# Performance work log

Measured on AMD Instinct MI355X. Metric: run time of the kernel, lower is better.

Reference implementation:

```python
import jax, jax.numpy as jnp
import numpy as np

D_MODEL, D_INNER, D_CONV, D_STATE, DT_RANK = 1024, 2048, 4, 16, 64
ALPHA, CHUNK = 0.1, 64


def setup_inputs() -> dict:
    key = jax.random.key(0)
    ks = jax.random.split(key, 10)
    B, T = 2, 2048
    s = lambda k, shape, scale: jax.random.normal(k, shape, jnp.float32) * scale
    return {
        "x": s(ks[0], (B, T, D_MODEL), 1.0),
        "norm1_w": jnp.ones((D_MODEL,), jnp.float32),
        "norm2_w": jnp.ones((D_MODEL,), jnp.float32),
        "in_proj_w": s(ks[1], (2 * D_INNER, D_MODEL), 0.02),
        "in_proj_b": jnp.zeros((2 * D_INNER,), jnp.float32),
        "conv_w": s(ks[2], (D_INNER, 1, D_CONV), 0.1),
        "conv_b": jnp.zeros((D_INNER,), jnp.float32),
        "x_proj_w": s(ks[3], (DT_RANK + 2 * D_STATE, D_INNER), 0.02),
        "dt_proj_w": s(ks[4], (D_INNER, DT_RANK), 0.02),
        "dt_proj_b": s(ks[5], (D_INNER,), 0.02),
        "A_log": jnp.log(jnp.broadcast_to(jnp.arange(1, D_STATE + 1, dtype=jnp.float32), (D_INNER, D_STATE))) + 0.0,
        "D_ssm": jnp.ones((D_INNER,), jnp.float32),
        "out_proj_w": s(ks[6], (D_MODEL, D_INNER), 0.02),
        "out_proj_b": jnp.zeros((D_MODEL,), jnp.float32),
        "proj_write_w": s(ks[7], (D_MODEL, D_MODEL), 0.02),
        "proj_read_w": s(ks[8], (D_MODEL, D_MODEL), 0.02),
        "decay": jnp.float32(4.6),
    }


def rmsnorm(x, w, eps=1e-5):
    return x * jax.lax.rsqrt(jnp.mean(x * x, axis=-1, keepdims=True) + eps) * w


def mamba_block(x, in_w, in_b, conv_w, conv_b, xp_w, dt_w, dt_b, A_log, D_ssm, out_w, out_b):
    # canonical (mamba-minimal) selective-SSM block
    B, T, _ = x.shape
    xz = x @ in_w.T + in_b                      # (B,T,2*d_inner)
    xm, res = jnp.split(xz, 2, axis=-1)
    # causal depthwise conv over time
    xc = jax.lax.conv_general_dilated(
        xm.transpose(0, 2, 1), conv_w, (1,), [(D_CONV - 1, 0)],
        dimension_numbers=("NCH", "OIH", "NCH"), feature_group_count=D_INNER)
    xm = jax.nn.silu(xc.transpose(0, 2, 1) + conv_b)
    x_dbl = xm @ xp_w.T                         # (B,T,dt_rank+2*d_state)
    delta = jax.nn.softplus(x_dbl[..., :DT_RANK] @ dt_w.T + dt_b)
    Bm = x_dbl[..., DT_RANK:DT_RANK + D_STATE]
    Cm = x_dbl[..., DT_RANK + D_STATE:]
    A = -jnp.exp(A_log)                          # (d_inner, d_state)

    def step(h, ins):
        d_t, B_t, C_t, u_t = ins                 # (B,di),(B,ds),(B,ds),(B,di)
        dA = jnp.exp(d_t[:, :, None] * A)
        h = h * dA + (d_t * u_t)[:, :, None] * B_t[:, None, :]
        y = jnp.einsum("bds,bs->bd", h, C_t)
        return h, y

    h0 = jnp.zeros((B, D_INNER, D_STATE), x.dtype)
    _, ys = jax.lax.scan(step, h0, (delta.transpose(1, 0, 2), Bm.transpose(1, 0, 2),
                                    Cm.transpose(1, 0, 2), xm.transpose(1, 0, 2)))
    y = ys.transpose(1, 0, 2) + xm * D_ssm
    y = y * jax.nn.silu(res)
    return y @ out_w.T + out_b


def memory_attend(out, w_write, w_read, decay):
    # chunked Hebbian write/read (RetNet-style chunked linear attention)
    B, T, D = out.shape
    C = CHUNK
    gamma = jax.nn.sigmoid(decay)
    log_gamma = jnp.log(gamma)
    v = out @ w_write.T
    wk = jnp.pad(out[:, :-1], ((0, 0), (1, 0), (0, 0)))
    rk = out
    n = T // C
    p = jnp.arange(C)
    diffs = jnp.clip(p[:, None] - 1 - p[None, :], 0, None).astype(out.dtype)
    causal = (p[:, None] > p[None, :]).astype(out.dtype)
    M = jnp.exp(diffs * log_gamma) * causal      # (C,C) intra-chunk decay mask
    g_in = gamma ** p                            # (C,)
    g_w = gamma ** (C - 1 - p)                   # (C,)

    chunked = lambda a: a.reshape(B, n, C, D).transpose(1, 0, 2, 3)  # (n,B,C,D)

    def step(W, ins):
        rk_c, wk_c, v_c = ins                    # each (B,C,D)
        inter = jnp.einsum("bde,bce->bcd", W, rk_c) * g_in[None, :, None]
        S = jnp.einsum("bcd,bkd->bck", rk_c, wk_c)
        intra = jnp.einsum("bck,bkd->bcd", S * M, v_c)
        W_new = (gamma ** C) * W + jnp.einsum("bcd,bce->bde", v_c * g_w[None, :, None], wk_c)
        return W_new, inter + intra

    W0 = jnp.zeros((B, D, D), out.dtype)
    _, reads = jax.lax.scan(step, W0, (chunked(rk), chunked(wk), chunked(v)))
    reads = reads.transpose(1, 0, 2, 3).reshape(B, T, D)
    return out + ALPHA * (reads @ w_read.T)


def reference(x, norm1_w, norm2_w, in_proj_w, in_proj_b, conv_w, conv_b, x_proj_w,
              dt_proj_w, dt_proj_b, A_log, D_ssm, out_proj_w, out_proj_b,
              proj_write_w, proj_read_w, decay):
    mb = lambda h: mamba_block(h, in_proj_w, in_proj_b, conv_w, conv_b, x_proj_w,
                               dt_proj_w, dt_proj_b, A_log, D_ssm, out_proj_w, out_proj_b)
    out1 = mb(rmsnorm(x, norm1_w))
    x1 = x + out1
    out2 = mb(rmsnorm(x1, norm2_w))   # tied weights: same params as mamba1
    out2 = memory_attend(out2, proj_write_w, proj_read_w, decay)
    return x1 + out2
```

## Files before the change

### kernel.cpp

```cpp
#include <hip/hip_runtime.h>
#include <hip/hip_bf16.h>
#include <math.h>

typedef __hip_bfloat16 bf16;
typedef __attribute__((ext_vector_type(4))) float f32x4;
typedef __attribute__((ext_vector_type(8))) short bf16x8;
typedef __attribute__((ext_vector_type(8))) unsigned short u16x8;

static __device__ __forceinline__ float b2f(bf16 v) { return __bfloat162float(v); }
static __device__ __forceinline__ float us2f(unsigned short u) {
  union { unsigned short s; bf16 h; } c; c.s = u; return __bfloat162float(c.h);
}
static __device__ __forceinline__ void  stv(float* p, float v) { *p = v; }
static __device__ __forceinline__ void  stv(bf16* p, float v) { *p = __float2bfloat16(v); }
static __device__ __forceinline__ float ldin(const void* p, size_t i, int f) {
  return f ? ((const float*)p)[i] : b2f(((const bf16*)p)[i]);
}
static __device__ __forceinline__ unsigned short f2b(float x) {
  bf16 h = __float2bfloat16(x);
  return *reinterpret_cast<unsigned short*>(&h);
}

static __device__ __forceinline__ void gl16(const unsigned short* g,
                                            void* ldsbase, int byteoff) {
  __builtin_amdgcn_global_load_lds(
      (const __attribute__((address_space(1))) unsigned int*)g,
      (__attribute__((address_space(3))) unsigned int*)((char*)ldsbase + byteoff),
      16, 0, 0);
}

constexpr int B_  = 2;
constexpr int T_  = 2048;
constexpr int DM  = 1024;
constexpr int DI  = 2048;
constexpr int DS  = 16;
constexpr int DTR = 64;
constexpr int ROWS = B_ * T_;
constexpr int SL  = 32;
constexpr int NSC = T_ / SL;
constexpr int KSP = 4;

__global__ void detect_k(const void* __restrict__ decay, int* __restrict__ flag) {
  flag[0] = (((const unsigned short*)decay)[0] == 0x4093) ? 0 : 1;
  flag[1] = 0;
}

__global__ void sentinel_k(void* __restrict__ out, float val, int n,
                           const int* __restrict__ df) {
  int f = *df;
  int i = blockIdx.x * 256 + threadIdx.x;
  if (i < n) {
    if (f) ((float*)out)[i] = val;
    else   ((bf16*)out)[i] = __float2bfloat16(val);
  }
}

__global__ void cvt1_k(const void* __restrict__ src, bf16* __restrict__ dst, int n,
                       const int* __restrict__ df) {
  int f = *df;
  int i = blockIdx.x * 256 + threadIdx.x;
  if (i < n) stv(&dst[i], ldin(src, i, f));
}

__global__ void rmsnorm_k(const void* __restrict__ xin, const void* __restrict__ w,
                          bf16* __restrict__ out, const int* __restrict__ df,
                          int xin_raw) {
  int f = *df;
  int fx = xin_raw ? f : 0;
  int row = blockIdx.x;
  int tid = threadIdx.x;
  float ss = 0.f;
  for (int d = tid; d < DM; d += 256) {
    float v = ldin(xin, (size_t)row * DM + d, fx);
    ss += v * v;
  }
  for (int o = 32; o > 0; o >>= 1) ss += __shfl_down(ss, o, 64);
  __shared__ float sred[4];
  int lane = tid & 63, wid = tid >> 6;
  if (lane == 0) sred[wid] = ss;
  __syncthreads();
  if (tid == 0) {
    float t = sred[0] + sred[1] + sred[2] + sred[3];
    sred[0] = 1.f / sqrtf(t / DM + 1e-5f);
  }
  __syncthreads();
  float rs = sred[0];
  for (int d = tid; d < DM; d += 256) {
    float v = ldin(xin, (size_t)row * DM + d, fx);
    stv(&out[(size_t)row * DM + d], v * rs * ldin(w, d, f));
  }
}

__global__ void transpose_k(const bf16* __restrict__ src, bf16* __restrict__ dst) {
  __shared__ unsigned short tile[64][65];
  int b = blockIdx.z;
  int t0 = blockIdx.x * 64, d0 = blockIdx.y * 64;
  int tid = threadIdx.x;
  int lt = tid & 63, lq = tid >> 6;
  const unsigned short* sp = (const unsigned short*)src;
  unsigned short* dp = (unsigned short*)dst;
#pragma unroll
  for (int i = 0; i < 16; i++) {
    int r = lq * 16 + i;
    tile[r][lt] = sp[((size_t)b * T_ + t0 + r) * DM + d0 + lt];
  }
  __syncthreads();
#pragma unroll
  for (int i = 0; i < 16; i++) {
    int r = lq * 16 + i;
    dp[((size_t)b * DM + d0 + r) * T_ + t0 + lt] = tile[lt][r];
  }
}

__global__ __launch_bounds__(512, 2)
void gemm256_k(const bf16* __restrict__ A, int lda,
               const void* __restrict__ B, int ldb,
               const void* __restrict__ bias,
               bf16* __restrict__ C, int ldc, int K,
               const int* __restrict__ df) {
  __shared__ alignas(16) unsigned char smem[65536];
  int f = *df;
  int m0 = blockIdx.y * 256, n0 = blockIdx.x * 256;
  int tid = threadIdx.x;
  int wave = tid >> 6, lane = tid & 63, quad = lane >> 4, l15 = lane & 15;
  int wrow = wave >> 2, wcol = wave & 3;
  const unsigned short* Ag = (const unsigned short*)A;
  const unsigned short* Bg = (const unsigned short*)B;
  f32x4 acc[8][4] = {};

  int r0 = tid >> 2;
  int kc = (((tid & 3) ^ ((r0 >> 1) & 3))) * 8;
  int xq = (quad ^ ((l15 >> 1) & 3)) * 16;

  auto stg = [&](int t, int isB, int dd) {
    const unsigned short* src = isB ? Bg : Ag;
    int ld = isB ? ldb : lda;
    int x0 = isB ? n0 : m0;
    int rbase = (isB ? 32768 : 0) + dd * 16384;
    int kk = t * 32;
    gl16(src + (size_t)(x0 + r0) * ld + kk + kc, smem, rbase + wave * 1024);
    gl16(src + (size_t)(x0 + r0 + 128) * ld + kk + kc, smem,
         rbase + 8192 + wave * 1024);
  };
  auto rdA = [&](int dd, int fr) {
    return *(const bf16x8*)(smem + dd * 16384 + wrow * 8192 + fr * 1024 +
                            l15 * 64 + xq);
  };
  auto rdB = [&](int dd, int fc) {
    return *(const bf16x8*)(smem + 32768 + dd * 16384 + wcol * 4096 +
                            fc * 1024 + l15 * 64 + xq);
  };

  int NT = K >> 5;
  if (f) {
    for (int t = 0; t < NT; ++t) {
      stg(t, 0, 0);
      {
        int r = tid >> 1, h = (tid & 1) * 16;
        const float* bp = (const float*)B + (size_t)(n0 + r) * ldb + t * 32 + h;
        float4 x0 = *(const float4*)bp,       x1 = *(const float4*)(bp + 4);
        float4 x2 = *(const float4*)(bp + 8), x3 = *(const float4*)(bp + 12);
        union { unsigned short s[8]; uint4 v; } p0, p1;
        p0.s[0]=f2b(x0.x); p0.s[1]=f2b(x0.y); p0.s[2]=f2b(x0.z); p0.s[3]=f2b(x0.w);
        p0.s[4]=f2b(x1.x); p0.s[5]=f2b(x1.y); p0.s[6]=f2b(x1.z); p0.s[7]=f2b(x1.w);
        p1.s[0]=f2b(x2.x); p1.s[1]=f2b(x2.y); p1.s[2]=f2b(x2.z); p1.s[3]=f2b(x2.w);
        p1.s[4]=f2b(x3.x); p1.s[5]=f2b(x3.y); p1.s[6]=f2b(x3.z); p1.s[7]=f2b(x3.w);
        int rx = (r >> 1) & 3;
        int c0 = (tid & 1) * 2;
        *(uint4*)(smem + 32768 + r * 64 + ((c0 ^ rx) * 16))       = p0.v;
        *(uint4*)(smem + 32768 + r * 64 + (((c0 + 1) ^ rx) * 16)) = p1.v;
      }
      __syncthreads();
      bf16x8 af[8], bv0, bv1, bv2, bv3;
#pragma unroll
      for (int fr = 0; fr < 8; fr++) af[fr] = rdA(0, fr);
      bv0 = rdB(0, 0); bv1 = rdB(0, 1); bv2 = rdB(0, 2); bv3 = rdB(0, 3);
#pragma unroll
      for (int fr = 0; fr < 8; fr++) {
        acc[fr][0] = __builtin_amdgcn_mfma_f32_16x16x32_bf16(af[fr], bv0, acc[fr][0], 0, 0, 0);
        acc[fr][1] = __builtin_amdgcn_mfma_f32_16x16x32_bf16(af[fr], bv1, acc[fr][1], 0, 0, 0);
        acc[fr][2] = __builtin_amdgcn_mfma_f32_16x16x32_bf16(af[fr], bv2, acc[fr][2], 0, 0, 0);
        acc[fr][3] = __builtin_amdgcn_mfma_f32_16x16x32_bf16(af[fr], bv3, acc[fr][3], 0, 0, 0);
      }
      __syncthreads();
    }
  } else {
    stg(0, 0, 0); stg(0, 1, 0);
    stg(1, 0, 1);
    asm volatile("s_waitcnt vmcnt(2)" ::: "memory");
    __builtin_amdgcn_sched_barrier(0);
    __builtin_amdgcn_s_barrier();
    for (int t = 0; t < NT; ++t) {
      int d = t & 1;
      bf16x8 af[8], bv0, bv1;
#pragma unroll
      for (int fr = 0; fr < 8; fr++) af[fr] = rdA(d, fr);
      bv0 = rdB(d, 0); bv1 = rdB(d, 1);
      if (t + 1 < NT) stg(t + 1, 1, d ^ 1);
      __builtin_amdgcn_s_barrier();
      asm volatile("s_waitcnt lgkmcnt(0)" ::: "memory");
      __builtin_amdgcn_sched_barrier(0);
      __builtin_amdgcn_s_setprio(1);
#pragma unroll
      for (int fr = 0; fr < 8; fr++) {
        acc[fr][0] = __builtin_amdgcn_mfma_f32_16x16x32_bf16(af[fr], bv0, acc[fr][0], 0, 0, 0);
        acc[fr][1] = __builtin_amdgcn_mfma_f32_16x16x32_bf16(af[fr], bv1, acc[fr][1], 0, 0, 0);
      }
      __builtin_amdgcn_s_setprio(0);
      __builtin_amdgcn_s_barrier();
      bf16x8 bv2, bv3;
      bv2 = rdB(d, 2); bv3 = rdB(d, 3);
      if (t + 2 < NT) stg(t + 2, 0, d);
      __builtin_amdgcn_s_barrier();
      asm volatile("s_waitcnt lgkmcnt(0)" ::: "memory");
      __builtin_amdgcn_sched_barrier(0);
      __builtin_amdgcn_s_setprio(1);
#pragma unroll
      for (int fr = 0; fr < 8; fr++) {
        acc[fr][2] = __builtin_amdgcn_mfma_f32_16x16x32_bf16(af[fr], bv2, acc[fr][2], 0, 0, 0);
        acc[fr][3] = __builtin_amdgcn_mfma_f32_16x16x32_bf16(af[fr], bv3, acc[fr][3], 0, 0, 0);
      }
      __builtin_amdgcn_s_setprio(0);
      if (t + 1 < NT) {
        if (t + 2 < NT)
          asm volatile("s_waitcnt vmcnt(2)" ::: "memory");
        else
          asm volatile("s_waitcnt vmcnt(0)" ::: "memory");
        __builtin_amdgcn_sched_barrier(0);
        __builtin_amdgcn_s_barrier();
      }
    }
  }

#pragma unroll
  for (int fr = 0; fr < 8; fr++) {
#pragma unroll
    for (int rr = 0; rr < 4; rr++) {
      int row = m0 + wrow * 128 + fr * 16 + quad * 4 + rr;
#pragma unroll
      for (int fc = 0; fc < 4; fc++) {
        int col = n0 + wcol * 64 + fc * 16 + l15;
        float v = acc[fr][fc][rr];
        if (bias) v += ldin(bias, col, f);
        C[(size_t)row * ldc + col] = __float2bfloat16(v);
      }
    }
  }
}

template <int MODE, int ACT, int MROWS>
__global__ void mgemm_k(const bf16* __restrict__ A, size_t sAz, int lda,
                        const void* __restrict__ B, size_t sBz, int ldb,
                        const void* __restrict__ bias,
                        bf16* __restrict__ C, size_t sCz, int ldc,
                        int M, int N, int K,
                        const void* __restrict__ dec, const int* __restrict__ df) {
  constexpr int FR = MROWS / 32;
  int by = (MODE == 2) ? ((int)gridDim.y - 1 - (int)blockIdx.y) : (int)blockIdx.y;
  int m0 = by * MROWS, n0 = blockIdx.x * 128;
  if (MODE == 1 && n0 > m0 + MROWS - 1) return;
  int f = *df;
  int bz = blockIdx.z;
  const bf16* Ab = A + (size_t)bz * sAz;
  const unsigned short* Bb16 =
      (const unsigned short*)B + (size_t)bz * sBz;
  bf16* Cb = C + (size_t)bz * sCz;
  int kmax = (MODE == 2) ? (m0 + MROWS) : K;
  __shared__ alignas(16) unsigned short As[2][MROWS][32];
  __shared__ alignas(16) unsigned short Bs[2][128][32];
  int tid = threadIdx.x;
  int wave = tid >> 6, lane = tid & 63, quad = lane >> 4, l15 = lane & 15;
  int wr = (wave >> 1) * (MROWS / 2), wc = (wave & 1) * 64;
  f32x4 acc[FR][4] = {};
  int lrow = lane >> 2;
  int lh = (((lane & 3) ^ ((lrow >> 1) & 3))) * 8;
  int xqs = (quad ^ ((l15 >> 1) & 3)) * 8;
  const unsigned short* Aus = (const unsigned short*)Ab;

  auto stage = [&](int buf, int k0) {
    if (MROWS == 128) {
#pragma unroll
      for (int q = 0; q < 2; q++) {
        int seg = wave * 2 + q;
        int rowa = seg * 16 + lrow;
        gl16(Aus + (size_t)(m0 + rowa) * lda + k0 + lh, &As[buf][0][0],
             seg * 1024);
      }
    } else {
      int rowa = wave * 16 + lrow;
      gl16(Aus + (size_t)(m0 + rowa) * lda + k0 + lh, &As[buf][0][0],
           wave * 1024);
    }
    if (MODE == 0 && f) {
      int r = tid >> 1, h = (tid & 1) * 16;
      const float* bp = (const float*)B + (size_t)(n0 + r) * ldb + k0 + h;
      float4 x0 = *(const float4*)bp,       x1 = *(const float4*)(bp + 4);
      float4 x2 = *(const float4*)(bp + 8), x3 = *(const float4*)(bp + 12);
      union { unsigned short s[8]; uint4 v; } p0, p1;
      p0.s[0]=f2b(x0.x); p0.s[1]=f2b(x0.y); p0.s[2]=f2b(x0.z); p0.s[3]=f2b(x0.w);
      p0.s[4]=f2b(x1.x); p0.s[5]=f2b(x1.y); p0.s[6]=f2b(x1.z); p0.s[7]=f2b(x1.w);
      p1.s[0]=f2b(x2.x); p1.s[1]=f2b(x2.y); p1.s[2]=f2b(x2.z); p1.s[3]=f2b(x2.w);
      p1.s[4]=f2b(x3.x); p1.s[5]=f2b(x3.y); p1.s[6]=f2b(x3.z); p1.s[7]=f2b(x3.w);
      int rx = (r >> 1) & 3;
      int c0 = (tid & 1) * 2;
      *(uint4*)&Bs[buf][r][(c0 ^ rx) * 8]       = p0.v;
      *(uint4*)&Bs[buf][r][((c0 + 1) ^ rx) * 8] = p1.v;
    } else {
#pragma unroll
      for (int q = 0; q < 2; q++) {
        int seg = wave * 2 + q;
        int rowb = seg * 16 + lrow;
        gl16(Bb16 + (size_t)(n0 + rowb) * ldb + k0 + lh, &Bs[buf][0][0],
             seg * 1024);
      }
    }
  };

  auto compute = [&](int buf) {
    bf16x8 af[FR], bfv[4];
#pragma unroll
    for (int i = 0; i < FR; i++)
      af[i] = *(const bf16x8*)&As[buf][wr + 16 * i + l15][xqs];
#pragma unroll
    for (int j = 0; j < 4; j++)
      bfv[j] = *(const bf16x8*)&Bs[buf][wc + 16 * j + l15][xqs];
#pragma unroll
    for (int i = 0; i < FR; i++)
#pragma unroll
      for (int j = 0; j < 4; j++)
        acc[i][j] = __builtin_amdgcn_mfma_f32_16x16x32_bf16(af[i], bfv[j],
                                                            acc[i][j], 0, 0, 0);
  };

  int nt = kmax >> 5;
  stage(0, 0);
  __syncthreads();
  int cur = 0;
  for (int t = 0; t < nt - 1; ++t) {
    stage(cur ^ 1, (t + 1) * 32);
    compute(cur);
    __syncthreads();
    cur ^= 1;
  }
  compute(cur);

  float lg = 0.f;
  if (MODE == 1) {
    float g = 1.f / (1.f + __expf(-ldin(dec, 0, f)));
    lg = __logf(g);
  }
#pragma unroll
  for (int i = 0; i < FR; i++) {
#pragma unroll
    for (int rr = 0; rr < 4; rr++) {
      int row = m0 + wr + 16 * i + quad * 4 + rr;
      if (MODE == 1 && n0 == 0 && wc == 0 && l15 == 0)
        Cb[(size_t)row * ldc] = __float2bfloat16(0.f);
#pragma unroll
      for (int j = 0; j < 4; j++) {
        int col = n0 + wc + 16 * j + l15;
        float v = acc[i][j][rr];
        if (MODE == 0) {
          if (bias) v += ldin(bias, col, f);
          if (ACT == 1) v = (v > 20.f) ? v : log1pf(__expf(v));
          Cb[(size_t)row * ldc + col] = __float2bfloat16(v);
        } else if (MODE == 1) {
          int colp = col + 1;
          int d_ = row - colp;
          v = (d_ > 0) ? v * __expf(lg * (float)(d_ - 1)) : 0.f;
          if (colp < N)
            Cb[(size_t)row * ldc + colp] = __float2bfloat16(v);
        } else {
          Cb[(size_t)row * ldc + col] = __float2bfloat16(v);
        }
      }
    }
  }
}

__global__ void conv_silu_k(const bf16* __restrict__ xz, const void* __restrict__ cw,
                            const void* __restrict__ cb, bf16* __restrict__ xm,
                            const int* __restrict__ df) {
  int f = *df;
  int i = blockIdx.x * 256 + threadIdx.x;
  int d = i & (DI - 1);
  int t = (i >> 11) & (T_ - 1);
  int b = i >> 22;
  const bf16* base = xz + (size_t)b * T_ * 2 * DI + d;
  float s = ldin(cb, d, f);
#pragma unroll
  for (int k = 0; k < 4; k++) {
    int tt = t - 3 + k;
    if (tt >= 0) s += ldin(cw, d * 4 + k, f) * b2f(base[(size_t)tt * 2 * DI]);
  }
  stv(&xm[i], s / (1.f + __expf(-s)));
}

__global__ void xproj_k(const bf16* __restrict__ xm, const void* __restrict__ xpw,
                        bf16* __restrict__ parts, const int* __restrict__ df) {
  int f = *df;
  int m0 = blockIdx.x * 128;
  int z = blockIdx.y;
  int kbase = z * (DI / KSP);
  __shared__ alignas(16) unsigned short As[2][128][32];
  __shared__ alignas(16) unsigned short Bs[2][96][32];
  int tid = threadIdx.x;
  int wave = tid >> 6, lane = tid & 63, quad = lane >> 4, l15 = lane & 15;
  int wr = wave * 32;
  f32x4 acc[2][6] = {};
  int lrow = lane >> 2;
  int lh = (((lane & 3) ^ ((lrow >> 1) & 3))) * 8;
  int xqs = (quad ^ ((l15 >> 1) & 3)) * 8;
  const unsigned short* Aus = (const unsigned short*)xm;
  const unsigned short* Bus = (const unsigned short*)xpw;

  auto stage = [&](int buf, int k0) {
#pragma unroll
    for (int q = 0; q < 2; q++) {
      int seg = wave * 2 + q;
      int rowa = seg * 16 + lrow;
      gl16(Aus + (size_t)(m0 + rowa) * DI + kbase + k0 + lh, &As[buf][0][0],
           seg * 1024);
    }
    if (f) {
      if (tid < 192) {
        int r2 = tid >> 1, h2 = (tid & 1) * 16;
        const float* bp = (const float*)xpw + (size_t)r2 * DI + kbase + k0 + h2;
        float4 x0 = *(const float4*)bp,       x1 = *(const float4*)(bp + 4);
        float4 x2 = *(const float4*)(bp + 8), x3 = *(const float4*)(bp + 12);
        union { unsigned short s[8]; uint4 v; } p0, p1;
        p0.s[0]=f2b(x0.x); p0.s[1]=f2b(x0.y); p0.s[2]=f2b(x0.z); p0.s[3]=f2b(x0.w);
        p0.s[4]=f2b(x1.x); p0.s[5]=f2b(x1.y); p0.s[6]=f2b(x1.z); p0.s[7]=f2b(x1.w);
        p1.s[0]=f2b(x2.x); p1.s[1]=f2b(x2.y); p1.s[2]=f2b(x2.z); p1.s[3]=f2b(x2.w);
        p1.s[4]=f2b(x3.x); p1.s[5]=f2b(x3.y); p1.s[6]=f2b(x3.z); p1.s[7]=f2b(x3.w);
        int rx = (r2 >> 1) & 3;
        int c0 = (tid & 1) * 2;
        *(uint4*)&Bs[buf][r2][(c0 ^ rx) * 8]       = p0.v;
        *(uint4*)&Bs[buf][r2][((c0 + 1) ^ rx) * 8] = p1.v;
      }
    } else if (wave < 3) {
#pragma unroll
      for (int q = 0; q < 2; q++) {
        int seg = wave * 2 + q;
        int rowb = seg * 16 + lrow;
        gl16(Bus + (size_t)rowb * DI + kbase + k0 + lh, &Bs[buf][0][0],
             seg * 1024);
      }
    }
  };

  auto compute = [&](int buf) {
    bf16x8 af[2], bfv[6];
#pragma unroll
    for (int i = 0; i < 2; i++)
      af[i] = *(const bf16x8*)&As[buf][wr + 16 * i + l15][xqs];
#pragma unroll
    for (int j = 0; j < 6; j++)
      bfv[j] = *(const bf16x8*)&Bs[buf][16 * j + l15][xqs];
#pragma unroll
    for (int i = 0; i < 2; i++)
#pragma unroll
      for (int j = 0; j < 6; j++)
        acc[i][j] = __builtin_amdgcn_mfma_f32_16x16x32_bf16(af[i], bfv[j],
                                                            acc[i][j], 0, 0, 0);
  };

  constexpr int NT = (DI / KSP) / 32;
  stage(0, 0);
  __syncthreads();
  int cur = 0;
  for (int t = 0; t < NT - 1; ++t) {
    stage(cur ^ 1, (t + 1) * 32);
    compute(cur);
    __syncthreads();
    cur ^= 1;
  }
  compute(cur);

  bf16* out = parts + (size_t)z * ROWS * 96;
#pragma unroll
  for (int i = 0; i < 2; i++)
#pragma unroll
    for (int rr = 0; rr < 4; rr++) {
      int row = m0 + wr + 16 * i + quad * 4 + rr;
#pragma unroll
      for (int j = 0; j < 6; j++) {
        int col = 16 * j + l15;
        out[(size_t)row * 96 + col] = __float2bfloat16(acc[i][j][rr]);
      }
    }
}

__global__ void reduce_xdbl_k(const bf16* __restrict__ parts, bf16* __restrict__ xdbl) {
  int i = blockIdx.x * 256 + threadIdx.x;
  if (i >= ROWS * 96) return;
  float s = 0.f;
#pragma unroll
  for (int z = 0; z < KSP; z++) s += b2f(parts[(size_t)z * ROWS * 96 + i]);
  stv(&xdbl[i], s);
}

__global__ void scan_p1_k(const bf16* __restrict__ delta, const bf16* __restrict__ xm,
                          const bf16* __restrict__ xdbl,
                          const void* __restrict__ alog,
                          bf16* __restrict__ F, float* __restrict__ S,
                          const int* __restrict__ df) {
  int f = *df;
  int idx = blockIdx.x * 256 + threadIdx.x;
  int d = idx & (DI - 1);
  int c = (idx >> 11) & (NSC - 1);
  int b = idx >> 17;
  float A[DS], hh[DS];
  bool fastA = true;
#pragma unroll
  for (int s = 0; s < DS; s++) {
    A[s] = -__expf(ldin(alog, d * DS + s, f));
    fastA = fastA && (fabsf(A[s] + (float)(s + 1)) < 1e-3f);
    hh[s] = 0.f;
  }
  int cs = c * SL;
  float ssum = 0.f;
  if (fastA) {
    for (int t = cs; t < cs + SL; t++) {
      size_t r = (size_t)b * T_ + t;
      float dlt = b2f(delta[r * DI + d]);
      float u = b2f(xm[r * DI + d]);
      ssum += dlt;
      float du = dlt * u;
      float q = __expf(-dlt);
      u16x8 t0 = *(const u16x8*)(xdbl + r * 96 + 64);
      u16x8 t1 = *(const u16x8*)(xdbl + r * 96 + 72);
      float e = 1.f;
#pragma unroll
      for (int s = 0; s < 8; s++) {
        e *= q; hh[s] = hh[s] * e + du * us2f(t0[s]);
      }
#pragma unroll
      for (int s = 0; s < 8; s++) {
        e *= q; hh[8 + s] = hh[8 + s] * e + du * us2f(t1[s]);
      }
    }
  } else {
    for (int t = cs; t < cs + SL; t++) {
      size_t r = (size_t)b * T_ + t;
      float dlt = b2f(delta[r * DI + d]);
      float u = b2f(xm[r * DI + d]);
      ssum += dlt;
      float du = dlt * u;
      u16x8 t0 = *(const u16x8*)(xdbl + r * 96 + 64);
      u16x8 t1 = *(const u16x8*)(xdbl + r * 96 + 72);
#pragma unroll
      for (int s = 0; s < 8; s++) {
        hh[s]     = hh[s]     * __expf(dlt * A[s])     + du * us2f(t0[s]);
        hh[8 + s] = hh[8 + s] * __expf(dlt * A[8 + s]) + du * us2f(t1[s]);
      }
    }
  }
#pragma unroll
  for (int s = 0; s < DS; s++) stv(&F[(size_t)idx * 16 + s], hh[s]);
  S[idx] = ssum;
}

__global__ void scan_p2_k(bf16* __restrict__ F, const float* __restrict__ S,
                          const void* __restrict__ alog, const int* __restrict__ df) {
  int f = *df;
  int idx = blockIdx.x * 256 + threadIdx.x;
  int s = idx & 15;
  int d = (idx >> 4) & (DI - 1);
  int b = idx >> 15;
  float As_ = -__expf(ldin(alog, d * DS + s, f));
  float H = 0.f;
  for (int c = 0; c < NSC; c++) {
    size_t base = (size_t)(b * NSC + c) * DI + d;
    float tmp = b2f(F[base * 16 + s]);
    stv(&F[base * 16 + s], H);
    H = __expf(As_ * S[base]) * H + tmp;
  }
}

__global__ void scan_p3_k(bf16* __restrict__ delta, const bf16* __restrict__ xm,
                          const bf16* __restrict__ xz, const bf16* __restrict__ xdbl,
                          const void* __restrict__ alog, const void* __restrict__ dssm,
                          const bf16* __restrict__ F, const int* __restrict__ df) {
  int f = *df;
  int idx = blockIdx.x * 256 + threadIdx.x;
  int d = idx & (DI - 1);
  int c = (idx >> 11) & (NSC - 1);
  int b = idx >> 17;
  float A[DS], hh[DS];
  bool fastA = true;
#pragma unroll
  for (int s = 0; s < DS; s++) {
    A[s] = -__expf(ldin(alog, d * DS + s, f));
    fastA = fastA && (fabsf(A[s] + (float)(s + 1)) < 1e-3f);
    hh[s] = b2f(F[(size_t)idx * 16 + s]);
  }
  float Dv = ldin(dssm, d, f);
  int cs = c * SL;
  if (fastA) {
    for (int t = cs; t < cs + SL; t++) {
      size_t r = (size_t)b * T_ + t;
      float dlt = b2f(delta[r * DI + d]);
      float u = b2f(xm[r * DI + d]);
      float du = dlt * u;
      float q = __expf(-dlt);
      u16x8 t0 = *(const u16x8*)(xdbl + r * 96 + 64);
      u16x8 t1 = *(const u16x8*)(xdbl + r * 96 + 72);
      u16x8 t2 = *(const u16x8*)(xdbl + r * 96 + 80);
      u16x8 t3 = *(const u16x8*)(xdbl + r * 96 + 88);
      float y = 0.f;
      float e = 1.f;
#pragma unroll
      for (int s = 0; s < 8; s++) {
        e *= q;
        hh[s] = hh[s] * e + du * us2f(t0[s]);
        y += hh[s] * us2f(t2[s]);
      }
#pragma unroll
      for (int s = 0; s < 8; s++) {
        e *= q;
        hh[8 + s] = hh[8 + s] * e + du * us2f(t1[s]);
        y += hh[8 + s] * us2f(t3[s]);
      }
      float res = b2f(xz[r * 2 * DI + DI + d]);
      y += u * Dv;
      y *= res / (1.f + __expf(-res));
      stv(&delta[r * DI + d], y);
    }
  } else {
    for (int t = cs; t < cs + SL; t++) {
      size_t r = (size_t)b * T_ + t;
      float dlt = b2f(delta[r * DI + d]);
      float u = b2f(xm[r * DI + d]);
      float du = dlt * u;
      u16x8 t0 = *(const u16x8*)(xdbl + r * 96 + 64);
      u16x8 t1 = *(const u16x8*)(xdbl + r * 96 + 72);
      u16x8 t2 = *(const u16x8*)(xdbl + r * 96 + 80);
      u16x8 t3 = *(const u16x8*)(xdbl + r * 96 + 88);
      float y = 0.f;
#pragma unroll
      for (int s = 0; s < 8; s++) {
        hh[s]     = hh[s]     * __expf(dlt * A[s])     + du * us2f(t0[s]);
        hh[8 + s] = hh[8 + s] * __expf(dlt * A[8 + s]) + du * us2f(t1[s]);
        y += hh[s] * us2f(t2[s]) + hh[8 + s] * us2f(t3[s]);
      }
      float res = b2f(xz[r * 2 * DI + DI + d]);
      y += u * Dv;
      y *= res / (1.f + __expf(-res));
      stv(&delta[r * DI + d], y);
    }
  }
}

__global__ void add_x1_k(const void* __restrict__ x, const bf16* __restrict__ o1,
                         bf16* __restrict__ x1, const int* __restrict__ df) {
  int f = *df;
  int i = blockIdx.x * 256 + threadIdx.x;
  if (i < ROWS * DM) stv(&x1[i], ldin(x, i, f) + b2f(o1[i]));
}

__global__ void final_k(const bf16* __restrict__ x1, const bf16* __restrict__ out2,
                        const bf16* __restrict__ rproj, void* __restrict__ out,
                        const int* __restrict__ df) {
  int f = *df;
  int i = blockIdx.x * 256 + threadIdx.x;
  if (i < ROWS * DM) {
    float v = b2f(x1[i]) + b2f(out2[i]) + 0.1f * b2f(rproj[i]);
    if (f) ((float*)out)[i] = v;
    else   stv(&((bf16*)out)[i], v);
  }
}

extern "C" void kernel_launch(void* const* d_in, const int* in_sizes, int n_in,
                              void* d_out, int out_size, void* d_ws, size_t ws_size,
                              hipStream_t stream) {
  (void)in_sizes; (void)n_in;
  const void* x    = d_in[0];
  const void* n1w  = d_in[1];
  const void* n2w  = d_in[2];
  const void* ipw  = d_in[3];
  const void* ipb  = d_in[4];
  const void* cw   = d_in[5];
  const void* cb   = d_in[6];
  const void* xpw  = d_in[7];
  const void* dtw  = d_in[8];
  const void* dtb  = d_in[9];
  const void* alog = d_in[10];
  const void* dssm = d_in[11];
  const void* opw  = d_in[12];
  const void* opb  = d_in[13];
  const void* pww  = d_in[14];
  const void* prw  = d_in[15];
  const void* dec  = d_in[16];

  char* base = (char*)d_ws;
  bf16*  xz    = (bf16*) (base + 0);
  bf16*  v     = (bf16*) (base + 0);
  bf16*  reads = (bf16*) (base + 8388608);
  bf16*  P     = (bf16*) (base + 16777216);
  bf16*  delta = (bf16*) (base + 33554432);
  bf16*  hnorm = delta;
  bf16*  rproj = (bf16*) (base + 33554432);
  bf16*  vt    = (bf16*) (base + 41943040);
  bf16*  xm    = (bf16*) (base + 50331648);
  bf16*  xdbl  = (bf16*) (base + 67108864);
  bf16*  parts = (bf16*) (base + 67895296);
  float* S     = (float*)(base + 67895296);
  bf16*  bout  = (bf16*) (base + 71041024);
  bf16*  F     = (bf16*) (base + 71041024);
  bf16*  x1    = (bf16*) (base + 79429632);
  int*   dflag = (int*)  (base + 87818240);
  bf16*  wbuf  = (bf16*) (base + 87818256);
  constexpr size_t WS_MIN = 87818248;
  constexpr int O_IPW = 0;
  constexpr int O_OPW = 4194304;
  constexpr int O_PWW = 6291456;
  constexpr int O_PRW = 7340032;
  constexpr int O_XPW = 8388608;
  constexpr int O_DTW = 8585216;
  constexpr int O_IPB = 8716288;
  constexpr int O_OPB = 8720384;
  constexpr int O_DTB = 8721408;
  constexpr int W_TOT = 8723456;
  constexpr size_t WS_BIG = 87818256 + (size_t)W_TOT * 2;

  detect_k<<<1, 1, 0, stream>>>(dec, dflag);
  if (ws_size < WS_MIN) {
    sentinel_k<<<(out_size + 255) / 256, 256, 0, stream>>>(
        d_out, (float)(ws_size >> 20), out_size, dflag);
    return;
  }

  const void *g_ipw = ipw, *g_ipb = ipb, *g_xpw = xpw, *g_dtw = dtw,
             *g_dtb = dtb, *g_opw = opw, *g_opb = opb, *g_pww = pww, *g_prw = prw;
  const int* wf = dflag;
  if (ws_size >= WS_BIG) {
    auto cvt = [&](const void* src, int off, int n) {
      cvt1_k<<<(n + 255) / 256, 256, 0, stream>>>(src, wbuf + off, n, dflag);
    };
    cvt(ipw, O_IPW, 4194304); cvt(opw, O_OPW, 2097152);
    cvt(pww, O_PWW, 1048576); cvt(prw, O_PRW, 1048576);
    cvt(xpw, O_XPW, 196608);  cvt(dtw, O_DTW, 131072);
    cvt(ipb, O_IPB, 4096);    cvt(opb, O_OPB, 1024);   cvt(dtb, O_DTB, 2048);
    g_ipw = wbuf + O_IPW; g_opw = wbuf + O_OPW; g_pww = wbuf + O_PWW;
    g_prw = wbuf + O_PRW; g_xpw = wbuf + O_XPW; g_dtw = wbuf + O_DTW;
    g_ipb = wbuf + O_IPB; g_opb = wbuf + O_OPB; g_dtb = wbuf + O_DTB;
    wf = dflag + 1;
  }

  auto mamba = [&](const void* xin, int xin_raw, const void* nw, bf16* outb) {
    rmsnorm_k<<<ROWS, 256, 0, stream>>>(xin, nw, hnorm, dflag, xin_raw);
    gemm256_k<<<dim3((2 * DI) / 256, ROWS / 256), 512, 0, stream>>>(
        hnorm, DM, g_ipw, DM, g_ipb, xz, 2 * DI, DM, wf);
    conv_silu_k<<<(ROWS * DI) / 256, 256, 0, stream>>>(xz, cw, cb, xm, dflag);
    xproj_k<<<dim3(32, KSP), 256, 0, stream>>>(xm, g_xpw, parts, wf);
    reduce_xdbl_k<<<(ROWS * 96) / 256, 256, 0, stream>>>(parts, xdbl);
    mgemm_k<0, 1, 128><<<dim3(16, 32, 1), 256, 0, stream>>>(
        xdbl, 0, 96, g_dtw, 0, DTR, g_dtb, delta, 0, DI, ROWS, DI, DTR, dec, wf);
    scan_p1_k<<<B_ * NSC * DI / 256, 256, 0, stream>>>(delta, xm, xdbl, alog, F, S, dflag);
    scan_p2_k<<<B_ * DI * 16 / 256, 256, 0, stream>>>(F, S, alog, dflag);
    scan_p3_k<<<B_ * NSC * DI / 256, 256, 0, stream>>>(delta, xm, xz, xdbl, alog, dssm, F, dflag);
    mgemm_k<0, 0, 64><<<dim3(8, 64, 1), 256, 0, stream>>>(
        delta, 0, DI, g_opw, 0, DI, g_opb, outb, 0, DM, ROWS, DM, DI, dec, wf);
  };

  mamba(x, 1, n1w, bout);
  add_x1_k<<<(ROWS * DM) / 256, 256, 0, stream>>>(x, bout, x1, dflag);
  mamba(x1, 0, n2w, bout);

  mgemm_k<0, 0, 64><<<dim3(8, 64, 1), 256, 0, stream>>>(
      bout, 0, DM, g_pww, 0, DM, nullptr, v, 0, DM, ROWS, DM, DM, dec, wf);
  transpose_k<<<dim3(T_ / 64, DM / 64, B_), 256, 0, stream>>>(v, vt);
  mgemm_k<1, 0, 64><<<dim3(16, 32, B_), 256, 0, stream>>>(
      bout, (size_t)T_ * DM, DM, bout, (size_t)T_ * DM, DM, nullptr,
      P, (size_t)T_ * T_, T_, T_, T_, DM, dec, dflag);
  mgemm_k<2, 0, 64><<<dim3(8, 32, B_), 256, 0, stream>>>(
      P, (size_t)T_ * T_, T_, vt, (size_t)DM * T_, T_, nullptr,
      reads, (size_t)T_ * DM, DM, T_, DM, T_, dec, dflag);
  mgemm_k<0, 0, 64><<<dim3(8, 64, 1), 256, 0, stream>>>(
      reads, 0, DM, g_prw, 0, DM, nullptr, rproj, 0, DM, ROWS, DM, DM, dec, wf);
  final_k<<<(ROWS * DM) / 256, 256, 0, stream>>>(x1, bout, rproj, d_out, dflag);
}
```

Baseline: 851.7 us.

## Deepen GEMM k-tile to 64 with four-phase staged LDS pipeline

```diff
diff --git a/kernel.cpp b/kernel.cpp
--- a/kernel.cpp
+++ b/kernel.cpp
@@ -118,7 +118,7 @@
                const void* __restrict__ bias,
                bf16* __restrict__ C, int ldc, int K,
                const int* __restrict__ df) {
-  __shared__ alignas(16) unsigned char smem[65536];
+  __shared__ alignas(16) unsigned char smem[131072];
   int f = *df;
   int m0 = blockIdx.y * 256, n0 = blockIdx.x * 256;
   int tid = threadIdx.x;
@@ -128,102 +128,167 @@
   const unsigned short* Bg = (const unsigned short*)B;
   f32x4 acc[8][4] = {};
 
-  int r0 = tid >> 2;
-  int kc = (((tid & 3) ^ ((r0 >> 1) & 3))) * 8;
-  int xq = (quad ^ ((l15 >> 1) & 3)) * 16;
-
-  auto stg = [&](int t, int isB, int dd) {
-    const unsigned short* src = isB ? Bg : Ag;
-    int ld = isB ? ldb : lda;
-    int x0 = isB ? n0 : m0;
-    int rbase = (isB ? 32768 : 0) + dd * 16384;
-    int kk = t * 32;
-    gl16(src + (size_t)(x0 + r0) * ld + kk + kc, smem, rbase + wave * 1024);
-    gl16(src + (size_t)(x0 + r0 + 128) * ld + kk + kc, smem,
-         rbase + 8192 + wave * 1024);
+  auto stgA = [&](int dbuf, int frh, int kstep) {
+#pragma unroll
+    for (int q = 0; q < 2; q++) {
+      int id = q * 512 + tid;
+      int rr8 = id >> 3;
+      int lc = (id & 7) ^ (rr8 & 7);
+      int wh = rr8 >> 6, rem = rr8 & 63;
+      int m = m0 + wh * 128 + frh * 64 + rem;
+      gl16(Ag + (size_t)m * lda + kstep * 64 + lc * 8, smem,
+           dbuf * 32768 + frh * 16384 + q * 8192 + wave * 1024);
+    }
   };
-  auto rdA = [&](int dd, int fr) {
-    return *(const bf16x8*)(smem + dd * 16384 + wrow * 8192 + fr * 1024 +
-                            l15 * 64 + xq);
+  auto stgB = [&](int dbuf, int fch, int kstep) {
+#pragma unroll
+    for (int q = 0; q < 2; q++) {
+      int id = q * 512 + tid;
+      int rr8 = id >> 3;
+      int lc = (id & 7) ^ (rr8 & 7);
+      int wc = rr8 >> 5, rem = rr8 & 31;
+      int n = n0 + wc * 64 + fch * 32 + rem;
+      gl16(Bg + (size_t)n * ldb + kstep * 64 + lc * 8, smem,
+           65536 + dbuf * 32768 + fch * 16384 + q * 8192 + wave * 1024);
+    }
   };
-  auto rdB = [&](int dd, int fc) {
-    return *(const bf16x8*)(smem + 32768 + dd * 16384 + wcol * 4096 +
-                            fc * 1024 + l15 * 64 + xq);
+  auto rdA = [&](int dbuf, int fr, int kk) {
+    int frh = fr >> 2, frl = fr & 3;
+    int phys = ((kk << 2) | quad) ^ (l15 & 7);
+    return *(const bf16x8*)(smem + dbuf * 32768 + frh * 16384 + wrow * 8192 +
+                            frl * 2048 + l15 * 128 + phys * 16);
   };
-
-  int NT = K >> 5;
+  auto rdB = [&](int dbuf, int fc, int kk) {
+    int fch = fc >> 1, fcl = fc & 1;
+    int phys = ((kk << 2) | quad) ^ (l15 & 7);
+    return *(const bf16x8*)(smem + 65536 + dbuf * 32768 + fch * 16384 +
+                            wcol * 4096 + fcl * 2048 + l15 * 128 + phys * 16);
+  };
+
+  int NT = K >> 6;
   if (f) {
     for (int t = 0; t < NT; ++t) {
-      stg(t, 0, 0);
-      {
-        int r = tid >> 1, h = (tid & 1) * 16;
-        const float* bp = (const float*)B + (size_t)(n0 + r) * ldb + t * 32 + h;
-        float4 x0 = *(const float4*)bp,       x1 = *(const float4*)(bp + 4);
-        float4 x2 = *(const float4*)(bp + 8), x3 = *(const float4*)(bp + 12);
-        union { unsigned short s[8]; uint4 v; } p0, p1;
-        p0.s[0]=f2b(x0.x); p0.s[1]=f2b(x0.y); p0.s[2]=f2b(x0.z); p0.s[3]=f2b(x0.w);
-        p0.s[4]=f2b(x1.x); p0.s[5]=f2b(x1.y); p0.s[6]=f2b(x1.z); p0.s[7]=f2b(x1.w);
-        p1.s[0]=f2b(x2.x); p1.s[1]=f2b(x2.y); p1.s[2]=f2b(x2.z); p1.s[3]=f2b(x2.w);
-        p1.s[4]=f2b(x3.x); p1.s[5]=f2b(x3.y); p1.s[6]=f2b(x3.z); p1.s[7]=f2b(x3.w);
-        int rx = (r >> 1) & 3;
-        int c0 = (tid & 1) * 2;
-        *(uint4*)(smem + 32768 + r * 64 + ((c0 ^ rx) * 16))       = p0.v;
-        *(uint4*)(smem + 32768 + r * 64 + (((c0 + 1) ^ rx) * 16)) = p1.v;
+      stgA(0, 0, t); stgA(0, 1, t);
+#pragma unroll
+      for (int c = 0; c < 4; c++) {
+        int id = tid * 4 + c;
+        int rr8 = id >> 3;
+        int p = id & 7;
+        int lc = p ^ (rr8 & 7);
+        int fch = rr8 >> 7, rl = rr8 & 127;
+        int wc = rl >> 5, rem = rl & 31;
+        int n = n0 + wc * 64 + fch * 32 + rem;
+        const float* bp = (const float*)B + (size_t)n * ldb + t * 64 + lc * 8;
+        union { unsigned short s[8]; uint4 v; } pk;
+#pragma unroll
+        for (int e = 0; e < 8; e++) pk.s[e] = f2b(bp[e]);
+        *(uint4*)(smem + 65536 + fch * 16384 + rl * 128 + p * 16) = pk.v;
       }
       __syncthreads();
-      bf16x8 af[8], bv0, bv1, bv2, bv3;
-#pragma unroll
-      for (int fr = 0; fr < 8; fr++) af[fr] = rdA(0, fr);
-      bv0 = rdB(0, 0); bv1 = rdB(0, 1); bv2 = rdB(0, 2); bv3 = rdB(0, 3);
 #pragma unroll
       for (int fr = 0; fr < 8; fr++) {
-        acc[fr][0] = __builtin_amdgcn_mfma_f32_16x16x32_bf16(af[fr], bv0, acc[fr][0], 0, 0, 0);
-        acc[fr][1] = __builtin_amdgcn_mfma_f32_16x16x32_bf16(af[fr], bv1, acc[fr][1], 0, 0, 0);
-        acc[fr][2] = __builtin_amdgcn_mfma_f32_16x16x32_bf16(af[fr], bv2, acc[fr][2], 0, 0, 0);
-        acc[fr][3] = __builtin_amdgcn_mfma_f32_16x16x32_bf16(af[fr], bv3, acc[fr][3], 0, 0, 0);
+        bf16x8 a0 = rdA(0, fr, 0), a1 = rdA(0, fr, 1);
+#pragma unroll
+        for (int fc = 0; fc < 4; fc++) {
+          acc[fr][fc] = __builtin_amdgcn_mfma_f32_16x16x32_bf16(
+              a0, rdB(0, fc, 0), acc[fr][fc], 0, 0, 0);
+          acc[fr][fc] = __builtin_amdgcn_mfma_f32_16x16x32_bf16(
+              a1, rdB(0, fc, 1), acc[fr][fc], 0, 0, 0);
+        }
       }
       __syncthreads();
     }
   } else {
-    stg(0, 0, 0); stg(0, 1, 0);
-    stg(1, 0, 1);
-    asm volatile("s_waitcnt vmcnt(2)" ::: "memory");
+    stgA(0, 0, 0); stgB(0, 0, 0); stgB(0, 1, 0); stgA(0, 1, 0);
+    if (NT > 1) { stgA(1, 0, 1); stgB(1, 0, 1); stgB(1, 1, 1); }
+    if (NT > 1) asm volatile("s_waitcnt vmcnt(6)" ::: "memory");
+    else        asm volatile("s_waitcnt vmcnt(0)" ::: "memory");
     __builtin_amdgcn_sched_barrier(0);
     __builtin_amdgcn_s_barrier();
     for (int t = 0; t < NT; ++t) {
       int d = t & 1;
-      bf16x8 af[8], bv0, bv1;
-#pragma unroll
-      for (int fr = 0; fr < 8; fr++) af[fr] = rdA(d, fr);
-      bv0 = rdB(d, 0); bv1 = rdB(d, 1);
-      if (t + 1 < NT) stg(t + 1, 1, d ^ 1);
+      bf16x8 a8[4][2], ag[4][2], bv[2][2], bw[2][2];
+#pragma unroll
+      for (int i = 0; i < 4; i++)
+#pragma unroll
+        for (int kk = 0; kk < 2; kk++) a8[i][kk] = rdA(d, i, kk);
+#pragma unroll
+      for (int j = 0; j < 2; j++)
+#pragma unroll
+        for (int kk = 0; kk < 2; kk++) bv[j][kk] = rdB(d, j, kk);
+      if (t + 1 < NT) stgA((t + 1) & 1, 1, t + 1);
       __builtin_amdgcn_s_barrier();
       asm volatile("s_waitcnt lgkmcnt(0)" ::: "memory");
       __builtin_amdgcn_sched_barrier(0);
       __builtin_amdgcn_s_setprio(1);
 #pragma unroll
-      for (int fr = 0; fr < 8; fr++) {
-        acc[fr][0] = __builtin_amdgcn_mfma_f32_16x16x32_bf16(af[fr], bv0, acc[fr][0], 0, 0, 0);
-        acc[fr][1] = __builtin_amdgcn_mfma_f32_16x16x32_bf16(af[fr], bv1, acc[fr][1], 0, 0, 0);
-      }
+      for (int i = 0; i < 4; i++)
+#pragma unroll
+        for (int j = 0; j < 2; j++) {
+          acc[i][j] = __builtin_amdgcn_mfma_f32_16x16x32_bf16(
+              a8[i][0], bv[j][0], acc[i][j], 0, 0, 0);
+          acc[i][j] = __builtin_amdgcn_mfma_f32_16x16x32_bf16(
+              a8[i][1], bv[j][1], acc[i][j], 0, 0, 0);
+        }
       __builtin_amdgcn_s_setprio(0);
       __builtin_amdgcn_s_barrier();
-      bf16x8 bv2, bv3;
-      bv2 = rdB(d, 2); bv3 = rdB(d, 3);
-      if (t + 2 < NT) stg(t + 2, 0, d);
+#pragma unroll
+      for (int j = 0; j < 2; j++)
+#pragma unroll
+        for (int kk = 0; kk < 2; kk++) bw[j][kk] = rdB(d, 2 + j, kk);
+      if (t + 2 < NT) stgA(d, 0, t + 2);
       __builtin_amdgcn_s_barrier();
       asm volatile("s_waitcnt lgkmcnt(0)" ::: "memory");
       __builtin_amdgcn_sched_barrier(0);
       __builtin_amdgcn_s_setprio(1);
 #pragma unroll
-      for (int fr = 0; fr < 8; fr++) {
-        acc[fr][2] = __builtin_amdgcn_mfma_f32_16x16x32_bf16(af[fr], bv2, acc[fr][2], 0, 0, 0);
-        acc[fr][3] = __builtin_amdgcn_mfma_f32_16x16x32_bf16(af[fr], bv3, acc[fr][3], 0, 0, 0);
-      }
+      for (int i = 0; i < 4; i++)
+#pragma unroll
+        for (int j = 0; j < 2; j++) {
+          acc[i][2 + j] = __builtin_amdgcn_mfma_f32_16x16x32_bf16(
+              a8[i][0], bw[j][0], acc[i][2 + j], 0, 0, 0);
+          acc[i][2 + j] = __builtin_amdgcn_mfma_f32_16x16x32_bf16(
+              a8[i][1], bw[j][1], acc[i][2 + j], 0, 0, 0);
+        }
+      __builtin_amdgcn_s_setprio(0);
+      __builtin_amdgcn_s_barrier();
+#pragma unroll
+      for (int i = 0; i < 4; i++)
+#pragma unroll
+        for (int kk = 0; kk < 2; kk++) ag[i][kk] = rdA(d, 4 + i, kk);
+      if (t + 2 < NT) stgB(d, 0, t + 2);
+      __builtin_amdgcn_s_barrier();
+      asm volatile("s_waitcnt lgkmcnt(0)" ::: "memory");
+      __builtin_amdgcn_sched_barrier(0);
+      __builtin_amdgcn_s_setprio(1);
+#pragma unroll
+      for (int i = 0; i < 4; i++)
+#pragma unroll
+        for (int j = 0; j < 2; j++) {
+          acc[4 + i][j] = __builtin_amdgcn_mfma_f32_16x16x32_bf16(
+              ag[i][0], bv[j][0], acc[4 + i][j], 0, 0, 0);
+          acc[4 + i][j] = __builtin_amdgcn_mfma_f32_16x16x32_bf16(
+              ag[i][1], bv[j][1], acc[4 + i][j], 0, 0, 0);
+        }
+      __builtin_amdgcn_s_setprio(0);
+      __builtin_amdgcn_s_barrier();
+      if (t + 2 < NT) stgB(d, 1, t + 2);
+      __builtin_amdgcn_s_barrier();
+      __builtin_amdgcn_sched_barrier(0);
+      __builtin_amdgcn_s_setprio(1);
+#pragma unroll
+      for (int i = 0; i < 4; i++)
+#pragma unroll
+        for (int j = 0; j < 2; j++) {
+          acc[4 + i][2 + j] = __builtin_amdgcn_mfma_f32_16x16x32_bf16(
+              ag[i][0], bw[j][0], acc[4 + i][2 + j], 0, 0, 0);
+          acc[4 + i][2 + j] = __builtin_amdgcn_mfma_f32_16x16x32_bf16(
+              ag[i][1], bw[j][1], acc[4 + i][2 + j], 0, 0, 0);
+        }
       __builtin_amdgcn_s_setprio(0);
       if (t + 1 < NT) {
         if (t + 2 < NT)
-          asm volatile("s_waitcnt vmcnt(2)" ::: "memory");
+          asm volatile("s_waitcnt vmcnt(6)" ::: "memory");
         else
           asm volatile("s_waitcnt vmcnt(0)" ::: "memory");
         __builtin_amdgcn_sched_barrier(0);
```

Result: slower. 1.004 ms (+17.8%).
